# Optimization experiments

Hardware: AMD Instinct MI355X
Metric: run time of the kernel (lower is better)

## Reference

```python
import jax, jax.numpy as jnp
import numpy as np

DIM = 1024
HEADS = 16
DIM_HEAD = DIM // HEADS  # 64
MAX_FREQ = 256


def rotate_half(x):
    # interleaved pairs: (..., d) -> rotate each (x1, x2) pair to (-x2, x1)
    x = x.reshape(*x.shape[:-1], -1, 2)
    x1, x2 = x[..., 0], x[..., 1]
    return jnp.stack([-x2, x1], axis=-1).reshape(*x.shape[:-2], -1)


def axial_freqs_2d(H, W, rot_dim, max_freq):
    # 'pixel' freqs: linspace(1, max_freq/2, n) * pi per axis; each axis gets rot_dim/2 rotary dims
    n = rot_dim // 4
    freqs = jnp.linspace(1.0, max_freq / 2.0, n, dtype=jnp.float32) * jnp.pi
    ph = jnp.linspace(-1.0, 1.0, H, dtype=jnp.float32)
    pw = jnp.linspace(-1.0, 1.0, W, dtype=jnp.float32)
    fh = jnp.repeat(ph[:, None] * freqs[None, :], 2, axis=-1)  # (H, rot_dim//2)
    fw = jnp.repeat(pw[:, None] * freqs[None, :], 2, axis=-1)  # (W, rot_dim//2)
    fh = jnp.broadcast_to(fh[:, None, :], (H, W, rot_dim // 2))
    fw = jnp.broadcast_to(fw[None, :, :], (H, W, rot_dim // 2))
    return jnp.concatenate([fh, fw], axis=-1)  # (H, W, rot_dim)


def setup_inputs() -> dict:
    key = jax.random.key(0)
    k1, k2, k3 = jax.random.split(key, 3)
    b, H, W = 8, 32, 32
    L = H * W
    x = jax.random.normal(k1, (b, L, DIM), dtype=jnp.float32)
    # torch Linear weights stored pre-transposed for direct x @ W
    w_qkv = jax.random.normal(k2, (DIM, 3 * DIM), dtype=jnp.float32) * (DIM ** -0.5)
    w_proj = jax.random.normal(k3, (DIM, DIM), dtype=jnp.float32) * (DIM ** -0.5)
    return {"x": x, "w_qkv": w_qkv, "w_proj": w_proj, "H": H, "W": W}


def reference(x, w_qkv, w_proj, H, W):
    b, L, d = x.shape
    qkv = x @ w_qkv  # (b, L, 3d)
    q, k, v = jnp.split(qkv, 3, axis=-1)

    def split_heads(t):
        return t.reshape(b, L, HEADS, DIM_HEAD)  # (b, L, h, dh)

    q, k, v = split_heads(q), split_heads(k), split_heads(v)

    # 2D axial RoPE over the full head dim (rope_use_dim == dim_head)
    freqs = axial_freqs_2d(H, W, DIM_HEAD, MAX_FREQ).reshape(L, DIM_HEAD)
    cos = jnp.cos(freqs)[None, :, None, :]  # (1, L, 1, dh)
    sin = jnp.sin(freqs)[None, :, None, :]
    q = q * cos + rotate_half(q) * sin
    k = k * cos + rotate_half(k) * sin

    # module pre-scales q by dh^-0.5 AND SDPA scales again by dh^-0.5 -> dh^-1 total (faithful)
    scale_total = 1.0 / DIM_HEAD
    scores = jnp.einsum('blhd,bmhd->bhlm', q, k) * scale_total  # (b, h, L, L)
    attn = jax.nn.softmax(scores, axis=-1)
    out = jnp.einsum('bhlm,bmhd->blhd', attn, v).reshape(b, L, d)
    return out @ w_proj
```

## Files before the change

### kernel.cpp

```cpp
#include <hip/hip_runtime.h>
#include <hip/hip_bf16.h>
#include <math.h>

typedef __bf16 bf16_t;
typedef __attribute__((ext_vector_type(8))) __bf16 bf16x8;
typedef __attribute__((ext_vector_type(4))) __bf16 bf16x4;
typedef __attribute__((ext_vector_type(4))) short s16x4;
typedef __attribute__((ext_vector_type(4))) float f32x4;

#define AS1C(p) ((const __attribute__((address_space(1))) void*)(p))
#define AS3(p)  ((__attribute__((address_space(3))) void*)(p))

__device__ __forceinline__ float fast_exp2(float x) { return __builtin_amdgcn_exp2f(x); }

__device__ __forceinline__ void tconv_body(const float* __restrict__ in,
                                           bf16_t* __restrict__ out, int R, int C,
                                           int r0, int c0, float (*tile)[65], int tid) {
#pragma unroll
    for (int i = 0; i < 16; ++i) {
        int e = i * 256 + tid;
        int r = e >> 6, c = e & 63;
        tile[r][c] = in[(size_t)(r0 + r) * C + c0 + c];
    }
    __syncthreads();
#pragma unroll
    for (int i = 0; i < 16; ++i) {
        int e = i * 256 + tid;
        int c = e >> 6, r = e & 63;
        out[(size_t)(c0 + c) * R + r0 + r] = (bf16_t)tile[r][c];
    }
}

__global__ __launch_bounds__(256) void k_prep(const float* __restrict__ x,
                                              const float* __restrict__ wqkv,
                                              const float* __restrict__ wproj,
                                              bf16_t* __restrict__ xb,
                                              bf16_t* __restrict__ wqT,
                                              bf16_t* __restrict__ wpT,
                                              float* __restrict__ cosT,
                                              float* __restrict__ sinT) {
    __shared__ float tile[64][65];
    const int bid = blockIdx.x, tid = threadIdx.x;
    if (bid < 8192) {
        int i = bid * 256 + tid;
        float4 v = reinterpret_cast<const float4*>(x)[i];
        bf16x4 o;
        o[0] = (bf16_t)v.x; o[1] = (bf16_t)v.y; o[2] = (bf16_t)v.z; o[3] = (bf16_t)v.w;
        reinterpret_cast<bf16x4*>(xb)[i] = o;
    } else if (bid < 8960) {
        int t = bid - 8192;
        tconv_body(wqkv, wqT, 1024, 3072, (t / 48) * 64, (t % 48) * 64, tile, tid);
    } else if (bid < 9216) {
        int t = bid - 8960;
        tconv_body(wproj, wpT, 1024, 1024, (t / 16) * 64, (t % 16) * 64, tile, tid);
    } else {
        int i = (bid - 9216) * 256 + tid;
        int l = i >> 6, d = i & 63;
        int hh = l >> 5, ww = l & 31;
        float pos = (d < 32) ? (-1.0f + (2.0f / 31.0f) * (float)hh)
                             : (-1.0f + (2.0f / 31.0f) * (float)ww);
        int fi = (d & 31) >> 1;
        float fb = (1.0f + (127.0f / 15.0f) * (float)fi) * 3.14159265358979323846f;
        float fr = pos * fb;
        cosT[i] = cosf(fr);
        sinT[i] = sinf(fr);
    }
}

__device__ __forceinline__ void gemm128_pipe(const bf16_t* __restrict__ A,
                                             const bf16_t* __restrict__ Bt,
                                             int rowA0, int colB0, int w, int l,
                                             bf16_t* As, bf16_t* Bs,
                                             f32x4 acc[4][4]) {
    const int wr = w >> 1, wc = w & 1;
    const int r8 = l >> 3;
    const int sc = ((l & 7) ^ r8) << 3;

#define STG8(buf, kt)                                                                      \
    {                                                                                      \
        _Pragma("unroll")                                                                  \
        for (int j = 0; j < 4; ++j) {                                                      \
            int rr = j * 32 + w * 8 + r8;                                                  \
            __builtin_amdgcn_global_load_lds(                                              \
                AS1C(A + (size_t)(rowA0 + rr) * 1024 + (kt) * 64 + sc),                    \
                AS3(As + (buf) * 8192 + (j * 32 + w * 8) * 64), 16, 0, 0);                 \
            __builtin_amdgcn_global_load_lds(                                              \
                AS1C(Bt + (size_t)(colB0 + rr) * 1024 + (kt) * 64 + sc),                   \
                AS3(Bs + (buf) * 8192 + (j * 32 + w * 8) * 64), 16, 0, 0);                 \
        }                                                                                  \
    }

    STG8(0, 0);
    for (int T = 0; T < 16; ++T) {
        if (T < 15) {
            STG8((T + 1) & 1, T + 1);
            asm volatile("s_waitcnt vmcnt(8)" ::: "memory");
        } else {
            asm volatile("s_waitcnt vmcnt(0)" ::: "memory");
        }
        __builtin_amdgcn_s_barrier();
        const bf16_t* cA = As + (T & 1) * 8192;
        const bf16_t* cB = Bs + (T & 1) * 8192;
#pragma unroll
        for (int kk = 0; kk < 2; ++kk) {
            const int ec = (kk * 32 + (l >> 4) * 8) ^ ((l & 7) << 3);
            bf16x8 af[4], bfr[4];
#pragma unroll
            for (int mm = 0; mm < 4; ++mm)
                af[mm] = *reinterpret_cast<const bf16x8*>(
                    cA + (wr * 64 + mm * 16 + (l & 15)) * 64 + ec);
#pragma unroll
            for (int n = 0; n < 4; ++n)
                bfr[n] = *reinterpret_cast<const bf16x8*>(
                    cB + (wc * 64 + n * 16 + (l & 15)) * 64 + ec);
            asm volatile("s_waitcnt lgkmcnt(0)" ::: "memory");
            __builtin_amdgcn_sched_barrier(0);
            __builtin_amdgcn_s_setprio(1);
#pragma unroll
            for (int mm = 0; mm < 4; ++mm)
#pragma unroll
                for (int n = 0; n < 4; ++n)
                    acc[mm][n] = __builtin_amdgcn_mfma_f32_16x16x32_bf16(af[mm], bfr[n],
                                                                         acc[mm][n], 0, 0, 0);
            __builtin_amdgcn_s_setprio(0);
        }
        __builtin_amdgcn_s_barrier();
    }
#undef STG8
}

__global__ __launch_bounds__(256, 2) void k_gemm_qkv(const bf16_t* __restrict__ A,
                                                     const bf16_t* __restrict__ Bt,
                                                     const float* __restrict__ cosT,
                                                     const float* __restrict__ sinT,
                                                     bf16_t* __restrict__ qb,
                                                     bf16_t* __restrict__ kb,
                                                     bf16_t* __restrict__ vb) {
    __shared__ alignas(128) char smem[65536];
    bf16_t* As = (bf16_t*)smem;
    bf16_t* Bs = (bf16_t*)(smem + 32768);
    const int tid = threadIdx.x, w = tid >> 6, l = tid & 63;
    const int wr = w >> 1, wc = w & 1;
    const int bid = blockIdx.x;
    const int xcd = bid & 7, idx = bid >> 3;
    const int by = (xcd >> 1) * 16 + (idx & 15);
    const int bx = (xcd & 1) * 12 + (idx >> 4);
    const int rowA0 = by * 128, colB0 = bx * 128;

    f32x4 acc[4][4] = {};
    gemm128_pipe(A, Bt, rowA0, colB0, w, l, As, Bs, acc);

    const int part = colB0 >> 10;
    if (part == 2) {
        __builtin_amdgcn_sched_barrier(0);
        __syncthreads();
        bf16_t* Tb = (bf16_t*)smem;
#pragma unroll
        for (int m = 0; m < 4; ++m)
#pragma unroll
            for (int n = 0; n < 4; ++n) {
                int cc = wc * 64 + n * 16 + (l & 15);
                int rr = wr * 64 + m * 16 + (l >> 4) * 4;
#pragma unroll
                for (int r = 0; r < 4; ++r)
                    Tb[cc * 136 + rr + r] = (bf16_t)acc[m][n][r];
            }
        __syncthreads();
        const int j = tid >> 1, half = tid & 1;
        const int c = colB0 + j;
        const int head = (c & 1023) >> 6, d = c & 63;
        const int bb = rowA0 >> 10, ll0 = rowA0 & 1023;
        bf16_t* dst = vb + (((size_t)bb * 16 + head) * 64 + d) * 1024 + ll0 + half * 64;
        const bf16_t* srcp = Tb + j * 136 + half * 64;
#pragma unroll
        for (int e = 0; e < 8; ++e)
            *reinterpret_cast<bf16x8*>(dst + e * 8) =
                *reinterpret_cast<const bf16x8*>(srcp + e * 8);
    } else {
        bf16_t* dstb = (part == 0) ? qb : kb;
        const float qscl = (part == 0) ? (1.4426950408889634f / 64.0f) : 1.0f;
#pragma unroll
        for (int m = 0; m < 4; ++m)
#pragma unroll
            for (int n = 0; n < 4; ++n) {
                const int c = colB0 + wc * 64 + n * 16 + (l & 15);
                const int head = (c & 1023) >> 6;
                const int d = c & 63;
                const int rbase = rowA0 + wr * 64 + m * 16 + (l >> 4) * 4;
#pragma unroll
                for (int r = 0; r < 4; ++r) {
                    int row = rbase + r;
                    int bb = row >> 10, ll = row & 1023;
                    float v0 = acc[m][n][r];
                    float vp = __shfl_xor(v0, 1, 64);
                    float cs = cosT[ll * 64 + d];
                    float sn = sinT[ll * 64 + d];
                    float res = (d & 1) ? fmaf(vp, sn, v0 * cs) : fmaf(-vp, sn, v0 * cs);
                    dstb[(((size_t)bb * 16 + head) * 1024 + ll) * 64 + d] = (bf16_t)(res * qscl);
                }
            }
    }
}

__global__ __launch_bounds__(256, 2) void k_gemm_out(const bf16_t* __restrict__ A,
                                                     const bf16_t* __restrict__ Bt,
                                                     float* __restrict__ out) {
    __shared__ alignas(128) char smem[65536];
    bf16_t* As = (bf16_t*)smem;
    bf16_t* Bs = (bf16_t*)(smem + 32768);
    const int tid = threadIdx.x, w = tid >> 6, l = tid & 63;
    const int wr = w >> 1, wc = w & 1;
    const int bid = blockIdx.x;
    const int xcd = bid & 7, idx = bid >> 3;
    const int by = (xcd >> 1) * 16 + (idx & 15);
    const int bx = (xcd & 1) * 4 + (idx >> 4);
    const int rowA0 = by * 128, colB0 = bx * 128;

    f32x4 acc[4][4] = {};
    gemm128_pipe(A, Bt, rowA0, colB0, w, l, As, Bs, acc);

#pragma unroll
    for (int m = 0; m < 4; ++m)
#pragma unroll
        for (int n = 0; n < 4; ++n) {
            int c = colB0 + wc * 64 + n * 16 + (l & 15);
            int rbase = rowA0 + wr * 64 + m * 16 + (l >> 4) * 4;
#pragma unroll
            for (int r = 0; r < 4; ++r)
                out[(size_t)(rbase + r) * 1024 + c] = acc[m][n][r];
        }
}

__global__ __launch_bounds__(256, 4) void k_attn(const bf16_t* __restrict__ qb,
                                                 const bf16_t* __restrict__ kb,
                                                 const bf16_t* __restrict__ vb,
                                                 bf16_t* __restrict__ ob) {
    __shared__ alignas(128) bf16_t Ks[2][64 * 64];
    __shared__ alignas(128) bf16_t Vs[2][64 * 64];
    const int tid = threadIdx.x, w = tid >> 6, l = tid & 63;
    const int g = l >> 4;
    const int bid = blockIdx.x;
    const int bs = (bid & 7) * 128 + (bid >> 3);
    const int bh = bs >> 3, bi = bh >> 4, h = bh & 15;
    const int q0 = (bs & 7) * 128;
    const bf16_t* qbase = qb + (size_t)bh * 1024 * 64;
    const bf16_t* kbase = kb + (size_t)bh * 1024 * 64;
    const bf16_t* vbase = vb + (size_t)bh * 64 * 1024;

    bf16x8 qf[2][2];
#pragma unroll
    for (int m = 0; m < 2; ++m) {
        int qrow = q0 + w * 32 + m * 16 + (l & 15);
#pragma unroll
        for (int kk = 0; kk < 2; ++kk)
            qf[m][kk] = *reinterpret_cast<const bf16x8*>(
                qbase + (size_t)qrow * 64 + kk * 32 + g * 8);
    }

    float l_run[2] = {0.f, 0.f};
    f32x4 o_acc[2][4] = {};

    const int srow = l >> 3;
    const int sc = 8 * ((l & 7) ^ srow);
#define STAGE(buf, kv0)                                                                   \
    {                                                                                     \
        _Pragma("unroll")                                                                 \
        for (int i = 0; i < 2; ++i) {                                                     \
            int rr = w * 16 + i * 8 + srow;                                               \
            __builtin_amdgcn_global_load_lds(AS1C(kbase + (size_t)((kv0) + rr) * 64 + sc),\
                                             AS3(&Ks[buf][(w * 16 + i * 8) * 64]), 16, 0, 0); \
            __builtin_amdgcn_global_load_lds(AS1C(vbase + (size_t)rr * 1024 + (kv0) + sc),\
                                             AS3(&Vs[buf][(w * 16 + i * 8) * 64]), 16, 0, 0); \
        }                                                                                 \
    }

    STAGE(0, 0);
    __syncthreads();

    const float SHIFT = 4.0f;
    int cur = 0;
    for (int t = 0; t < 16; ++t) {
        if (t < 15) STAGE(cur ^ 1, (t + 1) * 64);

        f32x4 sacc[2][4] = {};
#pragma unroll
        for (int kk = 0; kk < 2; ++kk)
#pragma unroll
            for (int n = 0; n < 4; ++n) {
                int rr = n * 16 + (l & 15);
                int ec = (kk * 32 + g * 8) ^ ((l & 7) << 3);
                bf16x8 kfr = *reinterpret_cast<const bf16x8*>(&Ks[cur][rr * 64 + ec]);
                sacc[0][n] = __builtin_amdgcn_mfma_f32_16x16x32_bf16(kfr, qf[0][kk], sacc[0][n], 0, 0, 0);
                sacc[1][n] = __builtin_amdgcn_mfma_f32_16x16x32_bf16(kfr, qf[1][kk], sacc[1][n], 0, 0, 0);
            }

        s16x4 pa[2][4];
#pragma unroll
        for (int m = 0; m < 2; ++m) {
            float lsum = 0.f;
#pragma unroll
            for (int n = 0; n < 4; ++n) {
                bf16x4 pb;
#pragma unroll
                for (int r = 0; r < 4; ++r) {
                    float pv = fast_exp2(sacc[m][n][r] - SHIFT);
                    lsum += pv;
                    pb[r] = (bf16_t)pv;
                }
                pa[m][n] = __builtin_bit_cast(s16x4, pb);
            }
            l_run[m] += lsum;
        }

        const char* vrow = (const char*)&Vs[cur][0] + (l & 15) * 128;
#pragma unroll
        for (int c = 0; c < 4; ++c) {
            int kvb = (c * 32 + g * 8) ^ ((l & 7) << 4);
#pragma unroll
            for (int nd = 0; nd < 4; ++nd) {
                s16x4 vf = *reinterpret_cast<const s16x4*>(vrow + nd * 2048 + kvb);
                o_acc[0][nd] = __builtin_amdgcn_mfma_f32_16x16x16bf16_1k(pa[0][c], vf, o_acc[0][nd], 0, 0, 0);
                o_acc[1][nd] = __builtin_amdgcn_mfma_f32_16x16x16bf16_1k(pa[1][c], vf, o_acc[1][nd], 0, 0, 0);
            }
        }
        __syncthreads();
        cur ^= 1;
    }

#pragma unroll
    for (int m = 0; m < 2; ++m) {
        float ls = l_run[m];
        ls += __shfl_xor(ls, 16, 64);
        ls += __shfl_xor(ls, 32, 64);
        float inv = 1.0f / ls;
#pragma unroll
        for (int r = 0; r < 4; ++r) {
            float c2 = __shfl(inv, (l & 48) | (g * 4 + r), 64);
            int row = q0 + w * 32 + m * 16 + g * 4 + r;
#pragma unroll
            for (int n = 0; n < 4; ++n)
                ob[((size_t)bi * 1024 + row) * 1024 + h * 64 + n * 16 + (l & 15)] =
                    (bf16_t)(o_acc[m][n][r] * c2);
        }
    }
#undef STAGE
}

extern "C" void kernel_launch(void* const* d_in, const int* in_sizes, int n_in,
                              void* d_out, int out_size, void* d_ws, size_t ws_size,
                              hipStream_t stream) {
    (void)in_sizes; (void)n_in; (void)out_size; (void)ws_size;
    const float* x     = (const float*)d_in[0];
    const float* wqkv  = (const float*)d_in[1];
    const float* wproj = (const float*)d_in[2];
    char* ws = (char*)d_ws;

    bf16_t* xb  = (bf16_t*)(ws);
    bf16_t* wqT = (bf16_t*)(ws + 16777216ull);
    bf16_t* wpT = (bf16_t*)(ws + 23068672ull);
    bf16_t* qb  = (bf16_t*)(ws + 25165824ull);
    bf16_t* kb  = (bf16_t*)(ws + 41943040ull);
    bf16_t* vb  = (bf16_t*)(ws + 58720256ull);
    bf16_t* ob  = (bf16_t*)(ws + 75497472ull);
    float*  cosT = (float*)(ws + 92274688ull);
    float*  sinT = (float*)(ws + 92536832ull);

    k_prep<<<9472, 256, 0, stream>>>(x, wqkv, wproj, xb, wqT, wpT, cosT, sinT);
    k_gemm_qkv<<<1536, 256, 0, stream>>>(xb, wqT, cosT, sinT, qb, kb, vb);
    k_attn<<<1024, 256, 0, stream>>>(qb, kb, vb, ob);
    k_gemm_out<<<512, 256, 0, stream>>>(ob, wpT, (float*)d_out);
}
```

Before: 152.9 us.

## Fuse fp32-to-bf16 conversion of x into the QKV GEMM A-tile load

Removes the separate pass that converted x to bf16 in the prep kernel. The QKV GEMM now loads fp32 x through registers, converts to bf16 and writes it swizzled into LDS, while B tiles keep the async global-to-LDS path in a double-buffered pipeline. This drops a 32MB read plus 16MB write pass, but each GEMM block now reads fp32 A, twice the bytes, and this is repeated across the 24 column blocks. It also adds register pressure and VALU conversion work inside the main loop.

```diff
diff --git a/kernel.cpp b/kernel.cpp
--- a/kernel.cpp
+++ b/kernel.cpp
@@ -31,30 +31,22 @@
     }
 }
 
-__global__ __launch_bounds__(256) void k_prep(const float* __restrict__ x,
-                                              const float* __restrict__ wqkv,
+__global__ __launch_bounds__(256) void k_prep(const float* __restrict__ wqkv,
                                               const float* __restrict__ wproj,
-                                              bf16_t* __restrict__ xb,
                                               bf16_t* __restrict__ wqT,
                                               bf16_t* __restrict__ wpT,
                                               float* __restrict__ cosT,
                                               float* __restrict__ sinT) {
     __shared__ float tile[64][65];
     const int bid = blockIdx.x, tid = threadIdx.x;
-    if (bid < 8192) {
-        int i = bid * 256 + tid;
-        float4 v = reinterpret_cast<const float4*>(x)[i];
-        bf16x4 o;
-        o[0] = (bf16_t)v.x; o[1] = (bf16_t)v.y; o[2] = (bf16_t)v.z; o[3] = (bf16_t)v.w;
-        reinterpret_cast<bf16x4*>(xb)[i] = o;
-    } else if (bid < 8960) {
-        int t = bid - 8192;
+    if (bid < 768) {
+        int t = bid;
         tconv_body(wqkv, wqT, 1024, 3072, (t / 48) * 64, (t % 48) * 64, tile, tid);
-    } else if (bid < 9216) {
-        int t = bid - 8960;
+    } else if (bid < 1024) {
+        int t = bid - 768;
         tconv_body(wproj, wpT, 1024, 1024, (t / 16) * 64, (t % 16) * 64, tile, tid);
     } else {
-        int i = (bid - 9216) * 256 + tid;
+        int i = (bid - 1024) * 256 + tid;
         int l = i >> 6, d = i & 63;
         int hh = l >> 5, ww = l & 31;
         float pos = (d < 32) ? (-1.0f + (2.0f / 31.0f) * (float)hh)
@@ -129,7 +121,7 @@
 #undef STG8
 }
 
-__global__ __launch_bounds__(256, 2) void k_gemm_qkv(const bf16_t* __restrict__ A,
+__global__ __launch_bounds__(256, 2) void k_gemm_qkv(const float* __restrict__ X,
                                                      const bf16_t* __restrict__ Bt,
                                                      const float* __restrict__ cosT,
                                                      const float* __restrict__ sinT,
@@ -146,9 +138,90 @@
     const int by = (xcd >> 1) * 16 + (idx & 15);
     const int bx = (xcd & 1) * 12 + (idx >> 4);
     const int rowA0 = by * 128, colB0 = bx * 128;
+    const int r8 = l >> 3;
+    const int sc = ((l & 7) ^ r8) << 3;
+    const float* xrow = X + (size_t)(rowA0 + w * 8 + r8) * 1024 + (l & 7) * 8;
+
+    float4 areg[8];
+#define LDA(kt)                                                                            \
+    {                                                                                      \
+        _Pragma("unroll")                                                                  \
+        for (int j = 0; j < 4; ++j) {                                                      \
+            const float4* p = reinterpret_cast<const float4*>(xrow + (size_t)j * 32768 + (kt) * 64); \
+            areg[j * 2] = p[0];                                                            \
+            areg[j * 2 + 1] = p[1];                                                        \
+        }                                                                                  \
+    }
+#define WRA(buf)                                                                           \
+    {                                                                                      \
+        _Pragma("unroll")                                                                  \
+        for (int j = 0; j < 4; ++j) {                                                      \
+            const float* a0 = reinterpret_cast<const float*>(&areg[j * 2]);                \
+            bf16x8 vv;                                                                     \
+            _Pragma("unroll")                                                              \
+            for (int e = 0; e < 8; ++e) vv[e] = (bf16_t)a0[e];                             \
+            *reinterpret_cast<bf16x8*>(As + (buf) * 8192 + (j * 32 + w * 8 + r8) * 64 + sc) = vv; \
+        }                                                                                  \
+    }
+#define LDB(buf, kt)                                                                       \
+    {                                                                                      \
+        _Pragma("unroll")                                                                  \
+        for (int j = 0; j < 4; ++j) {                                                      \
+            int rr = j * 32 + w * 8 + r8;                                                  \
+            __builtin_amdgcn_global_load_lds(                                              \
+                AS1C(Bt + (size_t)(colB0 + rr) * 1024 + (kt) * 64 + sc),                   \
+                AS3(Bs + (buf) * 8192 + (j * 32 + w * 8) * 64), 16, 0, 0);                 \
+        }                                                                                  \
+    }
 
     f32x4 acc[4][4] = {};
-    gemm128_pipe(A, Bt, rowA0, colB0, w, l, As, Bs, acc);
+
+    LDA(0);
+    WRA(0);
+    LDA(1);
+    LDB(0, 0);
+
+    for (int T = 0; T < 16; ++T) {
+        if (T < 15) {
+            LDB((T + 1) & 1, T + 1);
+            asm volatile("s_waitcnt vmcnt(4)" ::: "memory");
+            WRA((T + 1) & 1);
+            if (T < 14) LDA(T + 2);
+        } else {
+            asm volatile("s_waitcnt vmcnt(0)" ::: "memory");
+        }
+        asm volatile("s_waitcnt lgkmcnt(0)" ::: "memory");
+        __builtin_amdgcn_s_barrier();
+        const bf16_t* cA = As + (T & 1) * 8192;
+        const bf16_t* cB = Bs + (T & 1) * 8192;
+#pragma unroll
+        for (int kk = 0; kk < 2; ++kk) {
+            const int ec = (kk * 32 + (l >> 4) * 8) ^ ((l & 7) << 3);
+            bf16x8 af[4], bfr[4];
+#pragma unroll
+            for (int mm = 0; mm < 4; ++mm)
+                af[mm] = *reinterpret_cast<const bf16x8*>(
+                    cA + (wr * 64 + mm * 16 + (l & 15)) * 64 + ec);
+#pragma unroll
+            for (int n = 0; n < 4; ++n)
+                bfr[n] = *reinterpret_cast<const bf16x8*>(
+                    cB + (wc * 64 + n * 16 + (l & 15)) * 64 + ec);
+            asm volatile("s_waitcnt lgkmcnt(0)" ::: "memory");
+            __builtin_amdgcn_sched_barrier(0);
+            __builtin_amdgcn_s_setprio(1);
+#pragma unroll
+            for (int mm = 0; mm < 4; ++mm)
+#pragma unroll
+                for (int n = 0; n < 4; ++n)
+                    acc[mm][n] = __builtin_amdgcn_mfma_f32_16x16x32_bf16(af[mm], bfr[n],
+                                                                         acc[mm][n], 0, 0, 0);
+            __builtin_amdgcn_s_setprio(0);
+        }
+        __builtin_amdgcn_s_barrier();
+    }
+#undef LDA
+#undef WRA
+#undef LDB
 
     const int part = colB0 >> 10;
     if (part == 2) {
@@ -355,7 +428,6 @@
     const float* wproj = (const float*)d_in[2];
     char* ws = (char*)d_ws;
 
-    bf16_t* xb  = (bf16_t*)(ws);
     bf16_t* wqT = (bf16_t*)(ws + 16777216ull);
     bf16_t* wpT = (bf16_t*)(ws + 23068672ull);
     bf16_t* qb  = (bf16_t*)(ws + 25165824ull);
@@ -365,8 +437,8 @@
     float*  cosT = (float*)(ws + 92274688ull);
     float*  sinT = (float*)(ws + 92536832ull);
 
-    k_prep<<<9472, 256, 0, stream>>>(x, wqkv, wproj, xb, wqT, wpT, cosT, sinT);
-    k_gemm_qkv<<<1536, 256, 0, stream>>>(xb, wqT, cosT, sinT, qb, kb, vb);
+    k_prep<<<1280, 256, 0, stream>>>(wqkv, wproj, wqT, wpT, cosT, sinT);
+    k_gemm_qkv<<<1536, 256, 0, stream>>>(x, wqT, cosT, sinT, qb, kb, vb);
     k_attn<<<1024, 256, 0, stream>>>(qb, kb, vb, ob);
     k_gemm_out<<<512, 256, 0, stream>>>(ob, wpT, (float*)d_out);
 }
```

Result: slower. 167.5 us (+9.5%).

## Triple-buffer K/V tiles in attention with partial vmcnt waits

Applied to the files above, without the earlier changes.

Changes the attention kernel's K/V staging from double to triple buffering, prefetching two tiles ahead. Full __syncthreads is replaced by s_waitcnt vmcnt(4) plus a raw barrier, so one tile's loads can stay in flight across iterations. The softmax row-sum accumulation is also reassociated into a tree to shorten the dependency chain. In exchange LDS use rises from 32KB to 48KB per block and launch bounds drop from 4 to 3 blocks per CU, which may cut occupancy.

```diff
diff --git a/kernel.cpp b/kernel.cpp
--- a/kernel.cpp
+++ b/kernel.cpp
@@ -231,12 +231,12 @@
         }
 }
 
-__global__ __launch_bounds__(256, 4) void k_attn(const bf16_t* __restrict__ qb,
+__global__ __launch_bounds__(256, 3) void k_attn(const bf16_t* __restrict__ qb,
                                                  const bf16_t* __restrict__ kb,
                                                  const bf16_t* __restrict__ vb,
                                                  bf16_t* __restrict__ ob) {
-    __shared__ alignas(128) bf16_t Ks[2][64 * 64];
-    __shared__ alignas(128) bf16_t Vs[2][64 * 64];
+    __shared__ alignas(128) bf16_t Ks[3][64 * 64];
+    __shared__ alignas(128) bf16_t Vs[3][64 * 64];
     const int tid = threadIdx.x, w = tid >> 6, l = tid & 63;
     const int g = l >> 4;
     const int bid = blockIdx.x;
@@ -275,12 +275,17 @@
     }
 
     STAGE(0, 0);
-    __syncthreads();
+    STAGE(1, 64);
+    asm volatile("s_waitcnt vmcnt(4)" ::: "memory");
+    __builtin_amdgcn_s_barrier();
 
     const float SHIFT = 4.0f;
     int cur = 0;
     for (int t = 0; t < 16; ++t) {
-        if (t < 15) STAGE(cur ^ 1, (t + 1) * 64);
+        if (t < 14) {
+            int nb = cur + 2; if (nb >= 3) nb -= 3;
+            STAGE(nb, (t + 2) * 64);
+        }
 
         f32x4 sacc[2][4] = {};
 #pragma unroll
@@ -297,19 +302,20 @@
         s16x4 pa[2][4];
 #pragma unroll
         for (int m = 0; m < 2; ++m) {
-            float lsum = 0.f;
+            float part[4];
 #pragma unroll
             for (int n = 0; n < 4; ++n) {
                 bf16x4 pb;
-#pragma unroll
-                for (int r = 0; r < 4; ++r) {
-                    float pv = fast_exp2(sacc[m][n][r] - SHIFT);
-                    lsum += pv;
-                    pb[r] = (bf16_t)pv;
-                }
+                float p0 = fast_exp2(sacc[m][n][0] - SHIFT);
+                float p1 = fast_exp2(sacc[m][n][1] - SHIFT);
+                float p2 = fast_exp2(sacc[m][n][2] - SHIFT);
+                float p3 = fast_exp2(sacc[m][n][3] - SHIFT);
+                pb[0] = (bf16_t)p0; pb[1] = (bf16_t)p1;
+                pb[2] = (bf16_t)p2; pb[3] = (bf16_t)p3;
+                part[n] = (p0 + p1) + (p2 + p3);
                 pa[m][n] = __builtin_bit_cast(s16x4, pb);
             }
-            l_run[m] += lsum;
+            l_run[m] += (part[0] + part[1]) + (part[2] + part[3]);
         }
 
         const char* vrow = (const char*)&Vs[cur][0] + (l & 15) * 128;
@@ -323,8 +329,13 @@
                 o_acc[1][nd] = __builtin_amdgcn_mfma_f32_16x16x16bf16_1k(pa[1][c], vf, o_acc[1][nd], 0, 0, 0);
             }
         }
-        __syncthreads();
-        cur ^= 1;
+
+        if (t < 15) {
+            if (t < 14) asm volatile("s_waitcnt vmcnt(4)" ::: "memory");
+            else        asm volatile("s_waitcnt vmcnt(0)" ::: "memory");
+            __builtin_amdgcn_s_barrier();
+        }
+        cur += 1; if (cur >= 3) cur -= 3;
     }
 
 #pragma unroll
```

Result: no change. 155.6 us (+1.8%).

## Halve GEMM K-tile to 32 to shrink LDS and double occupancy

Applied to the files above, without the earlier changes.

The shared 128x128 GEMM pipeline now stages K in chunks of 32 instead of 64, with a new XOR swizzle for the narrower LDS rows. This halves LDS use to 32 KB per block, and launch bounds rise from 2 to 4 blocks per CU for both the QKV and output GEMMs. The V transpose epilogue is split into two passes over 64-column halves so it fits the smaller buffer. The trade-off is twice as many pipeline iterations and barriers per tile, with less MFMA work between each sync, and possible register pressure at the higher occupancy target.

```diff
diff --git a/kernel.cpp b/kernel.cpp
--- a/kernel.cpp
+++ b/kernel.cpp
@@ -67,78 +67,76 @@
     }
 }
 
-__device__ __forceinline__ void gemm128_pipe(const bf16_t* __restrict__ A,
+__device__ __forceinline__ void gemm128_bk32(const bf16_t* __restrict__ A,
                                              const bf16_t* __restrict__ Bt,
                                              int rowA0, int colB0, int w, int l,
                                              bf16_t* As, bf16_t* Bs,
                                              f32x4 acc[4][4]) {
     const int wr = w >> 1, wc = w & 1;
-    const int r8 = l >> 3;
-    const int sc = ((l & 7) ^ r8) << 3;
-
-#define STG8(buf, kt)                                                                      \
+    const int lr = l >> 2;
+    const int scnk = ((l & 3) ^ ((l >> 3) & 3)) << 3;
+
+#define STG(buf, kt)                                                                       \
     {                                                                                      \
         _Pragma("unroll")                                                                  \
-        for (int j = 0; j < 4; ++j) {                                                      \
-            int rr = j * 32 + w * 8 + r8;                                                  \
+        for (int i = 0; i < 2; ++i) {                                                      \
+            int rb = (w * 2 + i) * 16;                                                     \
             __builtin_amdgcn_global_load_lds(                                              \
-                AS1C(A + (size_t)(rowA0 + rr) * 1024 + (kt) * 64 + sc),                    \
-                AS3(As + (buf) * 8192 + (j * 32 + w * 8) * 64), 16, 0, 0);                 \
+                AS1C(A + (size_t)(rowA0 + rb + lr) * 1024 + (kt) * 32 + scnk),             \
+                AS3(As + (buf) * 4096 + rb * 32), 16, 0, 0);                               \
             __builtin_amdgcn_global_load_lds(                                              \
-                AS1C(Bt + (size_t)(colB0 + rr) * 1024 + (kt) * 64 + sc),                   \
-                AS3(Bs + (buf) * 8192 + (j * 32 + w * 8) * 64), 16, 0, 0);                 \
+                AS1C(Bt + (size_t)(colB0 + rb + lr) * 1024 + (kt) * 32 + scnk),            \
+                AS3(Bs + (buf) * 4096 + rb * 32), 16, 0, 0);                               \
         }                                                                                  \
     }
 
-    STG8(0, 0);
-    for (int T = 0; T < 16; ++T) {
-        if (T < 15) {
-            STG8((T + 1) & 1, T + 1);
-            asm volatile("s_waitcnt vmcnt(8)" ::: "memory");
+    const int ec = ((l >> 4) ^ ((l >> 1) & 3)) << 3;
+
+    STG(0, 0);
+    for (int T = 0; T < 32; ++T) {
+        if (T < 31) {
+            STG((T + 1) & 1, T + 1);
+            asm volatile("s_waitcnt vmcnt(4)" ::: "memory");
         } else {
             asm volatile("s_waitcnt vmcnt(0)" ::: "memory");
         }
         __builtin_amdgcn_s_barrier();
-        const bf16_t* cA = As + (T & 1) * 8192;
-        const bf16_t* cB = Bs + (T & 1) * 8192;
-#pragma unroll
-        for (int kk = 0; kk < 2; ++kk) {
-            const int ec = (kk * 32 + (l >> 4) * 8) ^ ((l & 7) << 3);
-            bf16x8 af[4], bfr[4];
-#pragma unroll
-            for (int mm = 0; mm < 4; ++mm)
-                af[mm] = *reinterpret_cast<const bf16x8*>(
-                    cA + (wr * 64 + mm * 16 + (l & 15)) * 64 + ec);
+        const bf16_t* cA = As + (T & 1) * 4096;
+        const bf16_t* cB = Bs + (T & 1) * 4096;
+        bf16x8 af[4], bfr[4];
+#pragma unroll
+        for (int mm = 0; mm < 4; ++mm)
+            af[mm] = *reinterpret_cast<const bf16x8*>(
+                cA + (wr * 64 + mm * 16 + (l & 15)) * 32 + ec);
+#pragma unroll
+        for (int n = 0; n < 4; ++n)
+            bfr[n] = *reinterpret_cast<const bf16x8*>(
+                cB + (wc * 64 + n * 16 + (l & 15)) * 32 + ec);
+        asm volatile("s_waitcnt lgkmcnt(0)" ::: "memory");
+        __builtin_amdgcn_sched_barrier(0);
+        __builtin_amdgcn_s_setprio(1);
+#pragma unroll
+        for (int mm = 0; mm < 4; ++mm)
 #pragma unroll
             for (int n = 0; n < 4; ++n)
-                bfr[n] = *reinterpret_cast<const bf16x8*>(
-                    cB + (wc * 64 + n * 16 + (l & 15)) * 64 + ec);
-            asm volatile("s_waitcnt lgkmcnt(0)" ::: "memory");
-            __builtin_amdgcn_sched_barrier(0);
-            __builtin_amdgcn_s_setprio(1);
-#pragma unroll
-            for (int mm = 0; mm < 4; ++mm)
-#pragma unroll
-                for (int n = 0; n < 4; ++n)
-                    acc[mm][n] = __builtin_amdgcn_mfma_f32_16x16x32_bf16(af[mm], bfr[n],
-                                                                         acc[mm][n], 0, 0, 0);
-            __builtin_amdgcn_s_setprio(0);
-        }
+                acc[mm][n] = __builtin_amdgcn_mfma_f32_16x16x32_bf16(af[mm], bfr[n],
+                                                                     acc[mm][n], 0, 0, 0);
+        __builtin_amdgcn_s_setprio(0);
         __builtin_amdgcn_s_barrier();
     }
-#undef STG8
-}
-
-__global__ __launch_bounds__(256, 2) void k_gemm_qkv(const bf16_t* __restrict__ A,
+#undef STG
+}
+
+__global__ __launch_bounds__(256, 4) void k_gemm_qkv(const bf16_t* __restrict__ A,
                                                      const bf16_t* __restrict__ Bt,
                                                      const float* __restrict__ cosT,
                                                      const float* __restrict__ sinT,
                                                      bf16_t* __restrict__ qb,
                                                      bf16_t* __restrict__ kb,
                                                      bf16_t* __restrict__ vb) {
-    __shared__ alignas(128) char smem[65536];
+    __shared__ alignas(128) char smem[32768];
     bf16_t* As = (bf16_t*)smem;
-    bf16_t* Bs = (bf16_t*)(smem + 32768);
+    bf16_t* Bs = (bf16_t*)(smem + 16384);
     const int tid = threadIdx.x, w = tid >> 6, l = tid & 63;
     const int wr = w >> 1, wc = w & 1;
     const int bid = blockIdx.x;
@@ -148,34 +146,39 @@
     const int rowA0 = by * 128, colB0 = bx * 128;
 
     f32x4 acc[4][4] = {};
-    gemm128_pipe(A, Bt, rowA0, colB0, w, l, As, Bs, acc);
+    gemm128_bk32(A, Bt, rowA0, colB0, w, l, As, Bs, acc);
 
     const int part = colB0 >> 10;
     if (part == 2) {
-        __builtin_amdgcn_sched_barrier(0);
-        __syncthreads();
         bf16_t* Tb = (bf16_t*)smem;
 #pragma unroll
-        for (int m = 0; m < 4; ++m)
-#pragma unroll
-            for (int n = 0; n < 4; ++n) {
-                int cc = wc * 64 + n * 16 + (l & 15);
-                int rr = wr * 64 + m * 16 + (l >> 4) * 4;
-#pragma unroll
-                for (int r = 0; r < 4; ++r)
-                    Tb[cc * 136 + rr + r] = (bf16_t)acc[m][n][r];
-            }
-        __syncthreads();
-        const int j = tid >> 1, half = tid & 1;
-        const int c = colB0 + j;
-        const int head = (c & 1023) >> 6, d = c & 63;
-        const int bb = rowA0 >> 10, ll0 = rowA0 & 1023;
-        bf16_t* dst = vb + (((size_t)bb * 16 + head) * 64 + d) * 1024 + ll0 + half * 64;
-        const bf16_t* srcp = Tb + j * 136 + half * 64;
-#pragma unroll
-        for (int e = 0; e < 8; ++e)
-            *reinterpret_cast<bf16x8*>(dst + e * 8) =
-                *reinterpret_cast<const bf16x8*>(srcp + e * 8);
+        for (int p = 0; p < 2; ++p) {
+            __builtin_amdgcn_sched_barrier(0);
+            __syncthreads();
+            if (wc == p) {
+#pragma unroll
+                for (int m = 0; m < 4; ++m)
+#pragma unroll
+                    for (int n = 0; n < 4; ++n) {
+                        int cc = n * 16 + (l & 15);
+                        int rr = wr * 64 + m * 16 + (l >> 4) * 4;
+#pragma unroll
+                        for (int r = 0; r < 4; ++r)
+                            Tb[cc * 136 + rr + r] = (bf16_t)acc[m][n][r];
+                    }
+            }
+            __syncthreads();
+            const int j = tid >> 2, qtr = tid & 3;
+            const int c = colB0 + p * 64 + j;
+            const int head = (c & 1023) >> 6, d = c & 63;
+            const int bb = rowA0 >> 10, ll0 = rowA0 & 1023;
+            bf16_t* dst = vb + (((size_t)bb * 16 + head) * 64 + d) * 1024 + ll0 + qtr * 32;
+            const bf16_t* srcp = Tb + j * 136 + qtr * 32;
+#pragma unroll
+            for (int e = 0; e < 4; ++e)
+                *reinterpret_cast<bf16x8*>(dst + e * 8) =
+                    *reinterpret_cast<const bf16x8*>(srcp + e * 8);
+        }
     } else {
         bf16_t* dstb = (part == 0) ? qb : kb;
         const float qscl = (part == 0) ? (1.4426950408889634f / 64.0f) : 1.0f;
@@ -202,12 +205,12 @@
     }
 }
 
-__global__ __launch_bounds__(256, 2) void k_gemm_out(const bf16_t* __restrict__ A,
+__global__ __launch_bounds__(256, 4) void k_gemm_out(const bf16_t* __restrict__ A,
                                                      const bf16_t* __restrict__ Bt,
                                                      float* __restrict__ out) {
-    __shared__ alignas(128) char smem[65536];
+    __shared__ alignas(128) char smem[32768];
     bf16_t* As = (bf16_t*)smem;
-    bf16_t* Bs = (bf16_t*)(smem + 32768);
+    bf16_t* Bs = (bf16_t*)(smem + 16384);
     const int tid = threadIdx.x, w = tid >> 6, l = tid & 63;
     const int wr = w >> 1, wc = w & 1;
     const int bid = blockIdx.x;
@@ -217,7 +220,7 @@
     const int rowA0 = by * 128, colB0 = bx * 128;
 
     f32x4 acc[4][4] = {};
-    gemm128_pipe(A, Bt, rowA0, colB0, w, l, As, Bs, acc);
+    gemm128_bk32(A, Bt, rowA0, colB0, w, l, As, Bs, acc);
 
 #pragma unroll
     for (int m = 0; m < 4; ++m)
```

Result: slower. 157.5 us (+3.0%).
